# Performance work log

Hardware: AMD Instinct MI355X
Metric: run time of the kernel (lower is better)

The kernel has to match this reference:

```python
import jax, jax.numpy as jnp
import numpy as np

EPS = 1e-08


def setup_inputs() -> dict:
    key = jax.random.key(0)
    k1, k2, k3 = jax.random.split(key, 3)
    B, T, IN, OUT = 32, 500, 2048, 1024
    x = jax.random.normal(k1, (B, T, IN), dtype=jnp.float32)
    # torch init: normal(mean=0, std=w_init_std*sqrt(1/input_shape))
    w = jax.random.normal(k2, (IN, OUT), dtype=jnp.float32) * np.sqrt(1.0 / IN)
    # b ~ N(1.0, 0.01), clamped >= 0
    b = jnp.clip(1.0 + 0.01 * jax.random.normal(k3, (OUT,), dtype=jnp.float32), 0.0, None)
    decay_m = jnp.array([0.6], dtype=jnp.float32)  # N(0.6, .01) clamped to [0,1]
    decay_s = jnp.array([0.9], dtype=jnp.float32)  # N(0.9, .01) clamped to [0,1]
    return {"x": x, "w": w, "b": b, "decay_m": decay_m, "decay_s": decay_s}


def reference(x, w, b, decay_m, decay_s):
    # x: [B, T, IN]; w: [IN, OUT]
    B, T, _ = x.shape
    OUT = w.shape[1]
    h = jnp.einsum('btc,cd->btd', x, w)          # [B, T, OUT]
    norm = jnp.sum(w * w, axis=0)                 # [OUT]
    dm = decay_m[0]
    ds = decay_s[0]
    inv_norm = 1.0 / (norm + EPS)
    zeros = jnp.zeros((B, OUT), dtype=x.dtype)
    # spk is never assigned a spike value in the original forward (spike_fn
    # is never applied), so it remains zero throughout.
    spk = zeros

    def step(carry, inp):
        M, S, E = carry
        E = dm * norm * (E + spk)                 # spk == 0 (faithful to source)
        M = dm * (M + inp)
        S = ds * (S + inp)
        mem = M - S - E
        mthr = mem * inv_norm - b                 # [B, OUT]
        return (M, S, E), mthr

    (_, _, _), spk_rec_t = jax.lax.scan(step, (zeros, zeros, zeros),
                                        jnp.swapaxes(h, 0, 1))  # [T, B, OUT]
    spk_rec = jnp.swapaxes(spk_rec_t, 0, 1)       # [B, T, OUT]
    loss = 0.5 * jnp.mean(spk_rec ** 2)
    return (spk_rec, loss)
```

## Files before the change

### kernel.cpp

```cpp
#include <hip/hip_runtime.h>


typedef __bf16 bf16x8 __attribute__((ext_vector_type(8)));
typedef __bf16 bf16x4 __attribute__((ext_vector_type(4)));
typedef float  f32x4  __attribute__((ext_vector_type(4)));

#define BDIM 32
#define TDIM 500
#define INDIM 2048
#define OUTDIM 1024
#define MROWS 16000
#define NCHUNK 25
#define CHLEN 20
#define OUT_ELEMS 16384000

__device__ __forceinline__ void gld_lds16(const void* g, void* l) {
    __builtin_amdgcn_global_load_lds(
        (const __attribute__((address_space(1))) unsigned int*)g,
        (__attribute__((address_space(3))) unsigned int*)l, 16, 0, 0);
}

__global__ void convert_x(const float* __restrict__ x, __bf16* __restrict__ xb) {
    size_t i = ((size_t)blockIdx.x * 256 + threadIdx.x) * 8;
    float4 a = *(const float4*)(x + i);
    float4 b = *(const float4*)(x + i + 4);
    bf16x8 o;
    o[0] = (__bf16)a.x; o[1] = (__bf16)a.y; o[2] = (__bf16)a.z; o[3] = (__bf16)a.w;
    o[4] = (__bf16)b.x; o[5] = (__bf16)b.y; o[6] = (__bf16)b.z; o[7] = (__bf16)b.w;
    *(bf16x8*)(xb + i) = o;
}

__global__ void transpose_w(const float* __restrict__ w, __bf16* __restrict__ wbt,
                            float* __restrict__ normAcc) {
    __shared__ float tile[32][33];
    __shared__ float red[8][33];
    const int tx = threadIdx.x;
    const int ty = threadIdx.y;
    const int d0 = blockIdx.x * 32;
    const int c0 = blockIdx.y * 32;
    float s = 0.f;
#pragma unroll
    for (int i = 0; i < 4; ++i) {
        int c = c0 + ty + i * 8;
        float v = w[(size_t)c * OUTDIM + d0 + tx];
        tile[ty + i * 8][tx] = v;
        s += v * v;
    }
    red[ty][tx] = s;
    __syncthreads();
#pragma unroll
    for (int i = 0; i < 4; ++i) {
        int d = d0 + ty + i * 8;
        wbt[(size_t)d * INDIM + c0 + tx] = (__bf16)tile[tx][ty + i * 8];
    }
    if (ty == 0) {
        float t = red[0][tx] + red[1][tx] + red[2][tx] + red[3][tx]
                + red[4][tx] + red[5][tx] + red[6][tx] + red[7][tx];
        atomicAdd(&normAcc[d0 + tx], t);
    }
}

__global__ __launch_bounds__(256, 2) void gemm_bf16(
    const __bf16* __restrict__ A,
    const __bf16* __restrict__ Bt,
    __bf16* __restrict__ H)
{
    constexpr int K = INDIM;
    __shared__ __align__(16) __bf16 As[128 * 64];
    __shared__ __align__(16) __bf16 Bs[256 * 64];

    const int tid  = threadIdx.x;
    const int wave = tid >> 6;
    const int lane = tid & 63;
    const int bm = blockIdx.y * 128;
    const int bn = blockIdx.x * 256;
    const int wn = wave * 64;

    const int srow8 = lane >> 3;
    const int sseg  = lane & 7;
    const int quad = lane >> 4;
    const int mrow = lane & 15;

    f32x4 acc[8][4] = {};

    for (int k0 = 0; k0 < K; k0 += 64) {
        __syncthreads();
#pragma unroll
        for (int g = 0; g < 4; ++g) {
            const int rbase = wave * 32 + g * 8;
            const int row   = rbase + srow8;
            const int q     = sseg ^ (row & 7);
            gld_lds16(A + (size_t)(bm + row) * K + k0 + q * 8, &As[rbase * 64]);
        }
#pragma unroll
        for (int g = 0; g < 8; ++g) {
            const int rbase = wave * 64 + g * 8;
            const int row   = rbase + srow8;
            const int q     = sseg ^ (row & 7);
            gld_lds16(Bt + (size_t)(bn + row) * K + k0 + q * 8, &Bs[rbase * 64]);
        }
        __syncthreads();

#pragma unroll
        for (int ks = 0; ks < 2; ++ks) {
            bf16x8 af[8], bfr[4];
#pragma unroll
            for (int i = 0; i < 8; ++i) {
                const int r = i * 16 + mrow;
                af[i] = *(const bf16x8*)&As[r * 64 + (((ks * 4 + quad) ^ (r & 7)) * 8)];
            }
#pragma unroll
            for (int j = 0; j < 4; ++j) {
                const int r = wn + j * 16 + mrow;
                bfr[j] = *(const bf16x8*)&Bs[r * 64 + (((ks * 4 + quad) ^ (r & 7)) * 8)];
            }
#pragma unroll
            for (int i = 0; i < 8; ++i)
#pragma unroll
                for (int j = 0; j < 4; ++j)
                    acc[i][j] = __builtin_amdgcn_mfma_f32_16x16x32_bf16(
                        af[i], bfr[j], acc[i][j], 0, 0, 0);
        }
    }

#pragma unroll
    for (int i = 0; i < 8; ++i)
#pragma unroll
        for (int j = 0; j < 4; ++j)
#pragma unroll
            for (int r = 0; r < 4; ++r) {
                const int R = bm + i * 16 + quad * 4 + r;
                const int C = bn + wn + j * 16 + mrow;
                H[(size_t)R * OUTDIM + C] = (__bf16)acc[i][j][r];
            }
}

__global__ void scan1(const __bf16* __restrict__ H,
                      f32x4* __restrict__ cM, f32x4* __restrict__ cS,
                      const float* __restrict__ dmp, const float* __restrict__ dsp) {
    const float dm = *dmp, ds = *dsp;
    const int c = blockIdx.x, b = blockIdx.y, tid = threadIdx.x;
    f32x4 M = {}, S = {};
    const __bf16* p = H + ((size_t)b * TDIM + c * CHLEN) * OUTDIM + tid * 4;
#pragma unroll 4
    for (int t = 0; t < CHLEN; ++t) {
        bf16x4 hv = *(const bf16x4*)(p + (size_t)t * OUTDIM);
        f32x4 h; h[0] = hv[0]; h[1] = hv[1]; h[2] = hv[2]; h[3] = hv[3];
        M = dm * (M + h);
        S = ds * (S + h);
    }
    const size_t idx = ((size_t)c * BDIM + b) * 256 + tid;
    cM[idx] = M;
    cS[idx] = S;
}

__global__ void scan2(float* __restrict__ cM, float* __restrict__ cS,
                      const float* __restrict__ dmp, const float* __restrict__ dsp) {
    const float dm = *dmp, ds = *dsp;
    float km = 1.f, ks = 1.f;
#pragma unroll
    for (int i = 0; i < CHLEN; ++i) { km *= dm; ks *= ds; }
    const int gid = blockIdx.x * 256 + threadIdx.x;
    const int b = gid >> 10, d = gid & 1023;
    float tM = 0.f, tS = 0.f;
    for (int c = 0; c < NCHUNK; ++c) {
        const size_t idx = (((size_t)c * BDIM + b) << 10) + d;
        float oM = cM[idx], oS = cS[idx];
        cM[idx] = tM; cS[idx] = tS;
        tM = km * tM + oM;
        tS = ks * tS + oS;
    }
}

__global__ void scan3(const __bf16* __restrict__ H,
                      const f32x4* __restrict__ cM, const f32x4* __restrict__ cS,
                      const float* __restrict__ normAcc, const float* __restrict__ bias,
                      const float* __restrict__ dmp, const float* __restrict__ dsp,
                      float* __restrict__ out, float* __restrict__ lossAcc,
                      unsigned* __restrict__ ticket) {
    const float dm = *dmp, ds = *dsp;
    const int c = blockIdx.x, b = blockIdx.y, tid = threadIdx.x;
    const size_t cidx = ((size_t)c * BDIM + b) * 256 + tid;
    f32x4 M = cM[cidx];
    f32x4 S = cS[cidx];
    f32x4 nv = *(const f32x4*)(normAcc + tid * 4);
    f32x4 inv;
    inv[0] = 1.f / (nv[0] + 1e-8f); inv[1] = 1.f / (nv[1] + 1e-8f);
    inv[2] = 1.f / (nv[2] + 1e-8f); inv[3] = 1.f / (nv[3] + 1e-8f);
    f32x4 bv = *(const f32x4*)(bias + tid * 4);

    const size_t rowbase = ((size_t)b * TDIM + c * CHLEN) * OUTDIM + tid * 4;
    const __bf16* p = H + rowbase;
    float* o = out + rowbase;
    float loss = 0.f;
#pragma unroll 4
    for (int t = 0; t < CHLEN; ++t) {
        bf16x4 hv = *(const bf16x4*)(p + (size_t)t * OUTDIM);
        f32x4 h; h[0] = hv[0]; h[1] = hv[1]; h[2] = hv[2]; h[3] = hv[3];
        M = dm * (M + h);
        S = ds * (S + h);
        f32x4 r = (M - S) * inv - bv;
        *(f32x4*)(o + (size_t)t * OUTDIM) = r;
        loss += r[0] * r[0] + r[1] * r[1] + r[2] * r[2] + r[3] * r[3];
    }
    __shared__ float red[256];
    red[tid] = loss;
    __syncthreads();
    for (int s = 128; s > 0; s >>= 1) {
        if (tid < s) red[tid] += red[tid + s];
        __syncthreads();
    }
    if (tid == 0) {
        atomicAdd(lossAcc, red[0]);
        __threadfence();
        unsigned t = atomicAdd(ticket, 1u);
        if (t == NCHUNK * BDIM - 1) {
            float total = atomicAdd(lossAcc, 0.0f);
            out[OUT_ELEMS] = 0.5f * total / (float)OUT_ELEMS;
        }
    }
}

#define OFF_H      ((size_t)0)
#define OFF_WBT    ((size_t)32768000)
#define OFF_NORM   ((size_t)36962304)
#define OFF_LOSS   ((size_t)36966400)
#define OFF_TICKET ((size_t)36966404)
#define OFF_CM     ((size_t)36966656)
#define OFF_CS     ((size_t)40243456)

extern "C" void kernel_launch(void* const* d_in, const int* in_sizes, int n_in,
                              void* d_out, int out_size, void* d_ws, size_t ws_size,
                              hipStream_t stream) {
    const float* x  = (const float*)d_in[0];
    const float* w  = (const float*)d_in[1];
    const float* bb = (const float*)d_in[2];
    const float* dm = (const float*)d_in[3];
    const float* ds = (const float*)d_in[4];

    char* ws = (char*)d_ws;
    __bf16*   H    = (__bf16*)(ws + OFF_H);
    __bf16*   WBT  = (__bf16*)(ws + OFF_WBT);
    float*    NORM = (float*)(ws + OFF_NORM);
    float*    LOSS = (float*)(ws + OFF_LOSS);
    unsigned* TICK = (unsigned*)(ws + OFF_TICKET);
    f32x4*    CM   = (f32x4*)(ws + OFF_CM);
    f32x4*    CS   = (f32x4*)(ws + OFF_CS);
    __bf16*   XB   = (__bf16*)d_out;
    float*    out  = (float*)d_out;

    hipMemsetAsync(ws + OFF_NORM, 0, 4096 + 256, stream);

    convert_x<<<16000, 256, 0, stream>>>(x, XB);
    transpose_w<<<dim3(32, 64), dim3(32, 8), 0, stream>>>(w, WBT, NORM);
    gemm_bf16<<<dim3(4, 125), 256, 0, stream>>>(XB, WBT, H);
    scan1<<<dim3(NCHUNK, BDIM), 256, 0, stream>>>(H, CM, CS, dm, ds);
    scan2<<<128, 256, 0, stream>>>((float*)CM, (float*)CS, dm, ds);
    scan3<<<dim3(NCHUNK, BDIM), 256, 0, stream>>>(H, CM, CS, NORM, bb, dm, ds,
                                                  out, LOSS, TICK);
}
```

Measured before the change: 335.0 us.

## Fuse fp32-to-bf16 conversion of x into GEMM A-tile loads, shrink tile to 128x128

Removes the separate convert_x kernel and instead loads fp32 x directly in the GEMM, converting to bf16 in registers before writing swizzled LDS. This saves a full write and reread of the bf16 copy of x. The GEMM tile shrinks from 128x256 to 128x128 with a 2x2 wave layout, occupancy hint rises to 3, and a 1D grid with grouped block remapping improves L2 reuse. The trade-off is that the A loads become synchronous register loads instead of async global-to-LDS, and each x tile is now read 8 times as fp32 instead of 4 times as bf16.

```diff
diff --git a/kernel.cpp b/kernel.cpp
--- a/kernel.cpp
+++ b/kernel.cpp
@@ -18,16 +18,6 @@
     __builtin_amdgcn_global_load_lds(
         (const __attribute__((address_space(1))) unsigned int*)g,
         (__attribute__((address_space(3))) unsigned int*)l, 16, 0, 0);
-}
-
-__global__ void convert_x(const float* __restrict__ x, __bf16* __restrict__ xb) {
-    size_t i = ((size_t)blockIdx.x * 256 + threadIdx.x) * 8;
-    float4 a = *(const float4*)(x + i);
-    float4 b = *(const float4*)(x + i + 4);
-    bf16x8 o;
-    o[0] = (__bf16)a.x; o[1] = (__bf16)a.y; o[2] = (__bf16)a.z; o[3] = (__bf16)a.w;
-    o[4] = (__bf16)b.x; o[5] = (__bf16)b.y; o[6] = (__bf16)b.z; o[7] = (__bf16)b.w;
-    *(bf16x8*)(xb + i) = o;
 }
 
 __global__ void transpose_w(const float* __restrict__ w, __bf16* __restrict__ wbt,
@@ -60,28 +50,36 @@
     }
 }
 
-__global__ __launch_bounds__(256, 2) void gemm_bf16(
-    const __bf16* __restrict__ A,
+__global__ __launch_bounds__(256, 3) void gemm_bf16(
+    const float*  __restrict__ X,
     const __bf16* __restrict__ Bt,
     __bf16* __restrict__ H)
 {
     constexpr int K = INDIM;
     __shared__ __align__(16) __bf16 As[128 * 64];
-    __shared__ __align__(16) __bf16 Bs[256 * 64];
+    __shared__ __align__(16) __bf16 Bs[128 * 64];
+
+    const int bid = blockIdx.x;
+    const int r8  = bid & 7;
+    const int s   = bid >> 3;
+    const int by  = (s >> 3) * 8 + r8;
+    const int bx  = s & 7;
+    if (by >= 125) return;
 
     const int tid  = threadIdx.x;
     const int wave = tid >> 6;
     const int lane = tid & 63;
-    const int bm = blockIdx.y * 128;
-    const int bn = blockIdx.x * 256;
-    const int wn = wave * 64;
+    const int bm = by * 128;
+    const int bn = bx * 128;
+    const int wm = (wave & 1) * 64;
+    const int wn = (wave >> 1) * 64;
 
     const int srow8 = lane >> 3;
-    const int sseg  = lane & 7;
+    const int soct  = lane & 7;
     const int quad = lane >> 4;
     const int mrow = lane & 15;
 
-    f32x4 acc[8][4] = {};
+    f32x4 acc[4][4] = {};
 
     for (int k0 = 0; k0 < K; k0 += 64) {
         __syncthreads();
@@ -89,24 +87,28 @@
         for (int g = 0; g < 4; ++g) {
             const int rbase = wave * 32 + g * 8;
             const int row   = rbase + srow8;
-            const int q     = sseg ^ (row & 7);
-            gld_lds16(A + (size_t)(bm + row) * K + k0 + q * 8, &As[rbase * 64]);
-        }
-#pragma unroll
-        for (int g = 0; g < 8; ++g) {
-            const int rbase = wave * 64 + g * 8;
-            const int row   = rbase + srow8;
-            const int q     = sseg ^ (row & 7);
+            const int q     = soct ^ (row & 7);
             gld_lds16(Bt + (size_t)(bn + row) * K + k0 + q * 8, &Bs[rbase * 64]);
         }
+#pragma unroll
+        for (int g = 0; g < 4; ++g) {
+            const int row = wave * 32 + g * 8 + srow8;
+            const float* gp = X + (size_t)(bm + row) * K + k0 + soct * 8;
+            float4 a = *(const float4*)gp;
+            float4 b = *(const float4*)(gp + 4);
+            bf16x8 o;
+            o[0] = (__bf16)a.x; o[1] = (__bf16)a.y; o[2] = (__bf16)a.z; o[3] = (__bf16)a.w;
+            o[4] = (__bf16)b.x; o[5] = (__bf16)b.y; o[6] = (__bf16)b.z; o[7] = (__bf16)b.w;
+            *(bf16x8*)&As[row * 64 + ((soct ^ (row & 7)) * 8)] = o;
+        }
         __syncthreads();
 
 #pragma unroll
         for (int ks = 0; ks < 2; ++ks) {
-            bf16x8 af[8], bfr[4];
-#pragma unroll
-            for (int i = 0; i < 8; ++i) {
-                const int r = i * 16 + mrow;
+            bf16x8 af[4], bfr[4];
+#pragma unroll
+            for (int i = 0; i < 4; ++i) {
+                const int r = wm + i * 16 + mrow;
                 af[i] = *(const bf16x8*)&As[r * 64 + (((ks * 4 + quad) ^ (r & 7)) * 8)];
             }
 #pragma unroll
@@ -115,7 +117,7 @@
                 bfr[j] = *(const bf16x8*)&Bs[r * 64 + (((ks * 4 + quad) ^ (r & 7)) * 8)];
             }
 #pragma unroll
-            for (int i = 0; i < 8; ++i)
+            for (int i = 0; i < 4; ++i)
 #pragma unroll
                 for (int j = 0; j < 4; ++j)
                     acc[i][j] = __builtin_amdgcn_mfma_f32_16x16x32_bf16(
@@ -124,12 +126,12 @@
     }
 
 #pragma unroll
-    for (int i = 0; i < 8; ++i)
+    for (int i = 0; i < 4; ++i)
 #pragma unroll
         for (int j = 0; j < 4; ++j)
 #pragma unroll
             for (int r = 0; r < 4; ++r) {
-                const int R = bm + i * 16 + quad * 4 + r;
+                const int R = bm + wm + i * 16 + quad * 4 + r;
                 const int C = bn + wn + j * 16 + mrow;
                 H[(size_t)R * OUTDIM + C] = (__bf16)acc[i][j][r];
             }
@@ -246,14 +248,12 @@
     unsigned* TICK = (unsigned*)(ws + OFF_TICKET);
     f32x4*    CM   = (f32x4*)(ws + OFF_CM);
     f32x4*    CS   = (f32x4*)(ws + OFF_CS);
-    __bf16*   XB   = (__bf16*)d_out;
     float*    out  = (float*)d_out;
 
     hipMemsetAsync(ws + OFF_NORM, 0, 4096 + 256, stream);
 
-    convert_x<<<16000, 256, 0, stream>>>(x, XB);
     transpose_w<<<dim3(32, 64), dim3(32, 8), 0, stream>>>(w, WBT, NORM);
-    gemm_bf16<<<dim3(4, 125), 256, 0, stream>>>(XB, WBT, H);
+    gemm_bf16<<<1024, 256, 0, stream>>>(x, WBT, H);
     scan1<<<dim3(NCHUNK, BDIM), 256, 0, stream>>>(H, CM, CS, dm, ds);
     scan2<<<128, 256, 0, stream>>>((float*)CM, (float*)CS, dm, ds);
     scan3<<<dim3(NCHUNK, BDIM), 256, 0, stream>>>(H, CM, CS, NORM, bb, dm, ds,
```

Measured after the change: 396.3 us. 1.18x slower.

## Fuse fp32-to-bf16 conversion of x into GEMM A-tile loading

Applied to the files above, without the earlier changes.

Removes the separate convert_x pass that wrote a bf16 copy of x. The GEMM now loads fp32 x directly into registers one k-tile ahead, converts it to bf16 and stores it into swizzled LDS. This saves a full read-write pass over x, but each GEMM block now reads fp32 A, so A traffic per tile doubles and is re-read by the 4 N-blocks. It also adds register pressure and synchronous register-staged loads in place of the async global_load_lds path.

```diff
diff --git a/kernel.cpp b/kernel.cpp
--- a/kernel.cpp
+++ b/kernel.cpp
@@ -18,16 +18,6 @@
     __builtin_amdgcn_global_load_lds(
         (const __attribute__((address_space(1))) unsigned int*)g,
         (__attribute__((address_space(3))) unsigned int*)l, 16, 0, 0);
-}
-
-__global__ void convert_x(const float* __restrict__ x, __bf16* __restrict__ xb) {
-    size_t i = ((size_t)blockIdx.x * 256 + threadIdx.x) * 8;
-    float4 a = *(const float4*)(x + i);
-    float4 b = *(const float4*)(x + i + 4);
-    bf16x8 o;
-    o[0] = (__bf16)a.x; o[1] = (__bf16)a.y; o[2] = (__bf16)a.z; o[3] = (__bf16)a.w;
-    o[4] = (__bf16)b.x; o[5] = (__bf16)b.y; o[6] = (__bf16)b.z; o[7] = (__bf16)b.w;
-    *(bf16x8*)(xb + i) = o;
 }
 
 __global__ void transpose_w(const float* __restrict__ w, __bf16* __restrict__ wbt,
@@ -61,7 +51,7 @@
 }
 
 __global__ __launch_bounds__(256, 2) void gemm_bf16(
-    const __bf16* __restrict__ A,
+    const float*  __restrict__ X,
     const __bf16* __restrict__ Bt,
     __bf16* __restrict__ H)
 {
@@ -77,28 +67,54 @@
     const int wn = wave * 64;
 
     const int srow8 = lane >> 3;
-    const int sseg  = lane & 7;
+    const int soct  = lane & 7;
     const int quad = lane >> 4;
     const int mrow = lane & 15;
 
+    const int arow = wave * 32 + srow8;
+
     f32x4 acc[8][4] = {};
+    float4 pa[4][2];
+
+#pragma unroll
+    for (int g = 0; g < 4; ++g) {
+        const float* gp = X + (size_t)(bm + arow + g * 8) * K + soct * 8;
+        pa[g][0] = *(const float4*)gp;
+        pa[g][1] = *(const float4*)(gp + 4);
+    }
 
     for (int k0 = 0; k0 < K; k0 += 64) {
         __syncthreads();
-#pragma unroll
-        for (int g = 0; g < 4; ++g) {
-            const int rbase = wave * 32 + g * 8;
-            const int row   = rbase + srow8;
-            const int q     = sseg ^ (row & 7);
-            gld_lds16(A + (size_t)(bm + row) * K + k0 + q * 8, &As[rbase * 64]);
-        }
+
 #pragma unroll
         for (int g = 0; g < 8; ++g) {
             const int rbase = wave * 64 + g * 8;
             const int row   = rbase + srow8;
-            const int q     = sseg ^ (row & 7);
+            const int q     = soct ^ (row & 7);
             gld_lds16(Bt + (size_t)(bn + row) * K + k0 + q * 8, &Bs[rbase * 64]);
         }
+
+#pragma unroll
+        for (int g = 0; g < 4; ++g) {
+            const int row = arow + g * 8;
+            bf16x8 o;
+            o[0] = (__bf16)pa[g][0].x; o[1] = (__bf16)pa[g][0].y;
+            o[2] = (__bf16)pa[g][0].z; o[3] = (__bf16)pa[g][0].w;
+            o[4] = (__bf16)pa[g][1].x; o[5] = (__bf16)pa[g][1].y;
+            o[6] = (__bf16)pa[g][1].z; o[7] = (__bf16)pa[g][1].w;
+            *(bf16x8*)&As[row * 64 + ((soct ^ (row & 7)) * 8)] = o;
+        }
+
+        if (k0 + 64 < K) {
+#pragma unroll
+            for (int g = 0; g < 4; ++g) {
+                const float* gp = X + (size_t)(bm + arow + g * 8) * K
+                                    + (k0 + 64) + soct * 8;
+                pa[g][0] = *(const float4*)gp;
+                pa[g][1] = *(const float4*)(gp + 4);
+            }
+        }
+
         __syncthreads();
 
 #pragma unroll
@@ -246,14 +262,12 @@
     unsigned* TICK = (unsigned*)(ws + OFF_TICKET);
     f32x4*    CM   = (f32x4*)(ws + OFF_CM);
     f32x4*    CS   = (f32x4*)(ws + OFF_CS);
-    __bf16*   XB   = (__bf16*)d_out;
     float*    out  = (float*)d_out;
 
     hipMemsetAsync(ws + OFF_NORM, 0, 4096 + 256, stream);
 
-    convert_x<<<16000, 256, 0, stream>>>(x, XB);
     transpose_w<<<dim3(32, 64), dim3(32, 8), 0, stream>>>(w, WBT, NORM);
-    gemm_bf16<<<dim3(4, 125), 256, 0, stream>>>(XB, WBT, H);
+    gemm_bf16<<<dim3(4, 125), 256, 0, stream>>>(x, WBT, H);
     scan1<<<dim3(NCHUNK, BDIM), 256, 0, stream>>>(H, CM, CS, dm, ds);
     scan2<<<128, 256, 0, stream>>>((float*)CM, (float*)CS, dm, ds);
     scan3<<<dim3(NCHUNK, BDIM), 256, 0, stream>>>(H, CM, CS, NORM, bb, dm, ds,
```

Measured after the change: 366.8 us. 9.5% more time.
